# Kernel tuning notes

Measured on AMD Instinct MI355X. Metric: run time of the kernel, lower is better.

## Reference

```python
import jax, jax.numpy as jnp
import numpy as np

NEG_SLOPE = 0.2

def leaky_relu(x):
    return jnp.where(x >= 0, x, NEG_SLOPE * x)

def conv1x1(x, w, b):
    # x: [n,c,h,w], w: [o,c], b: [o]
    return jnp.einsum('nchw,oc->nohw', x, w) + b[None, :, None, None]

def setup_inputs() -> dict:
    key = jax.random.key(0)
    ks = jax.random.split(key, 7)
    n, c, h, w = 4, 64, 80, 80
    scale = 1.0 / np.sqrt(c)
    return {
        'x': jax.random.normal(ks[0], (n, c, h, w), dtype=jnp.float32),
        'w1': jax.random.normal(ks[1], (c, c), dtype=jnp.float32) * scale,
        'b1': jax.random.normal(ks[2], (c,), dtype=jnp.float32) * 0.01,
        'w2': jax.random.normal(ks[3], (c, c), dtype=jnp.float32) * scale,
        'b2': jax.random.normal(ks[4], (c,), dtype=jnp.float32) * 0.01,
        'w3': jax.random.normal(ks[5], (c, c), dtype=jnp.float32) * scale,
        'b3': jax.random.normal(ks[6], (c,), dtype=jnp.float32) * 0.01,
    }

def reference(x, w1, b1, w2, b2, w3, b3):
    n, c, h, w = x.shape
    e1 = leaky_relu(conv1x1(x, w1, b1))  # [n,c,h,w]
    e2 = leaky_relu(conv1x1(x, w2, b2))
    asm = leaky_relu(conv1x1(x, w3, b3))
    # q: [n, hw, c]; k: [n, c, hw]
    q = e1.transpose(0, 2, 3, 1).reshape(n, h * w, c)
    k = e2.reshape(n, c, h * w)
    score = jax.nn.softmax(jnp.matmul(q, k), axis=2)  # [n, hw, hw]
    v = asm.reshape(n, c, h * w).transpose(0, 2, 1)   # [n, hw, c]
    out = jnp.matmul(score, v)                        # [n, hw, c]
    return out.transpose(0, 2, 1).reshape(n, c, h, w)
```

## Files before the change

kernel.cpp:

```cpp
#include <hip/hip_runtime.h>


typedef __attribute__((ext_vector_type(8))) unsigned short us8;
typedef __attribute__((ext_vector_type(4))) unsigned short us4;
typedef __attribute__((ext_vector_type(8))) __bf16 bf16x8;
typedef __attribute__((ext_vector_type(16))) float f32x16;

#define HW 6400
#define L2E 1.44269504088896340736f
#define SHIFT 32.0f
#define KS 4
#define ITERS 25

union V8 { us8 s; us4 h[2]; bf16x8 b; };

__device__ __forceinline__ unsigned short f32_to_bf16(float f) {
  unsigned u = __float_as_uint(f);
  u += 0x7fffu + ((u >> 16) & 1u);
  return (unsigned short)(u >> 16);
}
__device__ __forceinline__ float bf16_bits_to_f32(unsigned short u) {
  return __uint_as_float(((unsigned)u) << 16);
}
__device__ __forceinline__ bf16x8 ldsfrag(const unsigned short* p) {
  V8 r;
  r.h[0] = *(const us4*)p;
  r.h[1] = *(const us4*)(p + 4);
  return r.b;
}

__global__ __launch_bounds__(256, 4) void conv_kernel(
    const float* __restrict__ x,
    const float* __restrict__ w1, const float* __restrict__ b1,
    const float* __restrict__ w2, const float* __restrict__ b2,
    const float* __restrict__ w3, const float* __restrict__ b3,
    unsigned short* __restrict__ Qg, unsigned short* __restrict__ Kg,
    unsigned short* __restrict__ Vg) {
  __shared__ __align__(16) float xs[64 * 68];
  const int t = threadIdx.x;
  const int n = blockIdx.y;
  const int p0 = blockIdx.x * 64;
  const int k = blockIdx.z;

  {
    const int c = t >> 2, part = t & 3;
    const float* src = x + ((size_t)(n * 64 + c) * HW + p0 + part * 16);
    float* dst = xs + c * 68 + part * 16;
#pragma unroll
    for (int i = 0; i < 4; ++i)
      *(float4*)(dst + i * 4) = *(const float4*)(src + i * 4);
  }

  const float* wm = (k == 0) ? w1 : (k == 1) ? w2 : w3;
  const float* bm = (k == 0) ? b1 : (k == 1) ? b2 : b3;
  const int p = t & 63;
  const int cg = __builtin_amdgcn_readfirstlane(t >> 6);

  __syncthreads();

  float acc[16];
#pragma unroll
  for (int i = 0; i < 16; ++i) acc[i] = bm[cg * 16 + i];
#pragma unroll
  for (int c4 = 0; c4 < 16; ++c4) {
    const float xv0 = xs[(c4 * 4 + 0) * 68 + p];
    const float xv1 = xs[(c4 * 4 + 1) * 68 + p];
    const float xv2 = xs[(c4 * 4 + 2) * 68 + p];
    const float xv3 = xs[(c4 * 4 + 3) * 68 + p];
#pragma unroll
    for (int i = 0; i < 16; ++i) {
      const float4 wv = *(const float4*)(wm + (cg * 16 + i) * 64 + c4 * 4);
      acc[i] = fmaf(wv.x, xv0, acc[i]);
      acc[i] = fmaf(wv.y, xv1, acc[i]);
      acc[i] = fmaf(wv.z, xv2, acc[i]);
      acc[i] = fmaf(wv.w, xv3, acc[i]);
    }
  }
#pragma unroll
  for (int i = 0; i < 16; ++i)
    acc[i] = fmaxf(acc[i], 0.f) + 0.2f * fminf(acc[i], 0.f);

  if (k == 0) {
    unsigned short u[16];
#pragma unroll
    for (int i = 0; i < 16; ++i) u[i] = f32_to_bf16(acc[i] * L2E);
    unsigned short* dst = Qg + (size_t)(n * HW + p0 + p) * 64 + cg * 16;
    us8 a, b;
#pragma unroll
    for (int j = 0; j < 8; ++j) { a[j] = u[j]; b[j] = u[8 + j]; }
    *(us8*)dst = a;
    *(us8*)(dst + 8) = b;
  } else if (k == 1) {
    unsigned short u[16];
#pragma unroll
    for (int i = 0; i < 16; ++i) u[i] = f32_to_bf16(acc[i]);
    unsigned short* dst = Kg + (size_t)(n * HW + p0 + p) * 64 + cg * 16;
    us8 a, b;
#pragma unroll
    for (int j = 0; j < 8; ++j) { a[j] = u[j]; b[j] = u[8 + j]; }
    *(us8*)dst = a;
    *(us8*)(dst + 8) = b;
  } else {
#pragma unroll
    for (int i = 0; i < 16; ++i)
      Vg[(size_t)(n * 64 + cg * 16 + i) * HW + p0 + p] = f32_to_bf16(acc[i]);
  }
}

__global__ __launch_bounds__(256, 3) void attn_kernel(
    const unsigned short* __restrict__ Qg, const unsigned short* __restrict__ Kg,
    const unsigned short* __restrict__ Vg, float* __restrict__ Opart,
    float* __restrict__ Lpart) {
  __shared__ __align__(16) char smem[52224];
  unsigned short* Qs = (unsigned short*)smem;
  unsigned short* Ksh = (unsigned short*)(smem + 17408);
  unsigned short* Vsh = (unsigned short*)(smem + 26112);
  unsigned short* Ps = (unsigned short*)(smem + 34816);
  float* Ot = (float*)smem;

  const int t = threadIdx.x;
  const int w = t >> 6;
  const int lane = t & 63;
  const int l31 = lane & 31;
  const int lh = lane >> 5;
  const int nb = blockIdx.y;
  const int qb = blockIdx.x * 128;
  const int ks = blockIdx.z;
  const int key0 = ks * (HW / KS);

  {
    const unsigned short* src = Qg + (size_t)(nb * HW + qb) * 64 + t * 32;
    unsigned short* dst = Qs + (t >> 1) * 68 + (t & 1) * 32;
#pragma unroll
    for (int i = 0; i < 4; ++i) {
      V8 v; v.s = *(const us8*)(src + i * 8);
      *(us4*)(dst + i * 8) = v.h[0];
      *(us4*)(dst + i * 8 + 4) = v.h[1];
    }
  }
  __syncthreads();

  bf16x8 aQ[4];
#pragma unroll
  for (int kst = 0; kst < 4; ++kst)
    aQ[kst] = ldsfrag(Qs + (w * 32 + l31) * 68 + kst * 16 + lh * 8);

  f32x16 accO[2];
#pragma unroll
  for (int ci = 0; ci < 2; ++ci)
#pragma unroll
    for (int r = 0; r < 16; ++r) accO[ci][r] = 0.f;
  float lpart = 0.f;

  const unsigned short* kbase = Kg + (size_t)nb * HW * 64;
  const unsigned short* vbase = Vg + (size_t)nb * 64 * HW;

  V8 kr0, kr1, vr0, vr1;
  {
    const unsigned short* ksrc = kbase + (size_t)(key0)*64 + t * 16;
    kr0.s = *(const us8*)ksrc;
    kr1.s = *(const us8*)(ksrc + 8);
    const unsigned short* vsrc = vbase + (size_t)(t >> 2) * HW + key0 + (t & 3) * 16;
    vr0.s = *(const us8*)vsrc;
    vr1.s = *(const us8*)(vsrc + 8);
  }

#pragma unroll 1
  for (int jt = 0; jt < ITERS; ++jt) {
    __syncthreads();
    {
      unsigned short* kdst = Ksh + (t >> 2) * 68 + (t & 3) * 16;
      *(us4*)(kdst) = kr0.h[0];
      *(us4*)(kdst + 4) = kr0.h[1];
      *(us4*)(kdst + 8) = kr1.h[0];
      *(us4*)(kdst + 12) = kr1.h[1];
      unsigned short* vdst = Vsh + (t >> 2) * 68 + (t & 3) * 16;
      *(us4*)(vdst) = vr0.h[0];
      *(us4*)(vdst + 4) = vr0.h[1];
      *(us4*)(vdst + 8) = vr1.h[0];
      *(us4*)(vdst + 12) = vr1.h[1];
    }
    __syncthreads();

    if (jt + 1 < ITERS) {
      const unsigned short* ksrc =
          kbase + (size_t)(key0 + (jt + 1) * 64) * 64 + t * 16;
      kr0.s = *(const us8*)ksrc;
      kr1.s = *(const us8*)(ksrc + 8);
      const unsigned short* vsrc =
          vbase + (size_t)(t >> 2) * HW + key0 + (jt + 1) * 64 + (t & 3) * 16;
      vr0.s = *(const us8*)vsrc;
      vr1.s = *(const us8*)(vsrc + 8);
    }

    f32x16 sacc[2];
#pragma unroll
    for (int ni = 0; ni < 2; ++ni)
#pragma unroll
      for (int r = 0; r < 16; ++r) sacc[ni][r] = 0.f;
#pragma unroll
    for (int kst = 0; kst < 4; ++kst) {
      const bf16x8 aK0 = ldsfrag(Ksh + l31 * 68 + kst * 16 + lh * 8);
      const bf16x8 aK1 = ldsfrag(Ksh + (32 + l31) * 68 + kst * 16 + lh * 8);
      sacc[0] = __builtin_amdgcn_mfma_f32_32x32x16_bf16(aK0, aQ[kst], sacc[0], 0, 0, 0);
      sacc[1] = __builtin_amdgcn_mfma_f32_32x32x16_bf16(aK1, aQ[kst], sacc[1], 0, 0, 0);
    }

    unsigned short* prow = Ps + (w * 32 + l31) * 68;
#pragma unroll
    for (int ni = 0; ni < 2; ++ni) {
#pragma unroll
      for (int q = 0; q < 4; ++q) {
        us4 pk;
#pragma unroll
        for (int j = 0; j < 4; ++j) {
          const float pv = __builtin_amdgcn_exp2f(sacc[ni][4 * q + j] - SHIFT);
          const unsigned short u = f32_to_bf16(pv);
          lpart += bf16_bits_to_f32(u);
          pk[j] = u;
        }
        *(us4*)(prow + ni * 32 + 8 * q + 4 * lh) = pk;
      }
    }

#pragma unroll
    for (int kst = 0; kst < 4; ++kst) {
      const bf16x8 ap = ldsfrag(Ps + (w * 32 + l31) * 68 + kst * 16 + lh * 8);
      const bf16x8 bv0 = ldsfrag(Vsh + l31 * 68 + kst * 16 + lh * 8);
      const bf16x8 bv1 = ldsfrag(Vsh + (32 + l31) * 68 + kst * 16 + lh * 8);
      accO[0] = __builtin_amdgcn_mfma_f32_32x32x16_bf16(ap, bv0, accO[0], 0, 0, 0);
      accO[1] = __builtin_amdgcn_mfma_f32_32x32x16_bf16(ap, bv1, accO[1], 0, 0, 0);
    }
  }

  const float lsum = lpart + __shfl_xor(lpart, 32);
  if (lh == 0)
    Lpart[((size_t)ks * 4 + nb) * HW + qb + w * 32 + l31] = lsum;

  __syncthreads();
#pragma unroll
  for (int ci = 0; ci < 2; ++ci)
#pragma unroll
    for (int r = 0; r < 16; ++r)
      Ot[(ci * 32 + l31) * 132 + w * 32 + 4 * lh + (r & 3) + 8 * (r >> 2)] =
          accO[ci][r];
  __syncthreads();
  {
    const int ch = t >> 2, part = t & 3;
    const float* src = Ot + ch * 132 + part * 32;
    float* dst = Opart + ((size_t)ks * 4 + nb) * (64 * HW) + (size_t)ch * HW +
                 qb + part * 32;
#pragma unroll
    for (int i = 0; i < 8; ++i)
      *(float4*)(dst + i * 4) = *(const float4*)(src + i * 4);
  }
}

__global__ __launch_bounds__(256) void combine_kernel(
    const float* __restrict__ Opart, const float* __restrict__ Lpart,
    float* __restrict__ out) {
  const int tid = blockIdx.x * 256 + threadIdx.x;
  const size_t e = (size_t)tid * 4;
  float4 o = {0.f, 0.f, 0.f, 0.f};
#pragma unroll
  for (int ks = 0; ks < KS; ++ks) {
    const float4 v = *(const float4*)(Opart + (size_t)ks * (4 * 64 * HW) + e);
    o.x += v.x; o.y += v.y; o.z += v.z; o.w += v.w;
  }
  const int n = (int)(e / (64 * HW));
  const int p = (int)(e % HW);
  float4 l = {0.f, 0.f, 0.f, 0.f};
#pragma unroll
  for (int ks = 0; ks < KS; ++ks) {
    const float4 v = *(const float4*)(Lpart + ((size_t)ks * 4 + n) * HW + p);
    l.x += v.x; l.y += v.y; l.z += v.z; l.w += v.w;
  }
  float4 r;
  r.x = o.x / l.x; r.y = o.y / l.y; r.z = o.z / l.z; r.w = o.w / l.w;
  *(float4*)(out + e) = r;
}

extern "C" void kernel_launch(void* const* d_in, const int* in_sizes, int n_in,
                              void* d_out, int out_size, void* d_ws, size_t ws_size,
                              hipStream_t stream) {
  const float* x = (const float*)d_in[0];
  const float* w1 = (const float*)d_in[1];
  const float* b1 = (const float*)d_in[2];
  const float* w2 = (const float*)d_in[3];
  const float* b2 = (const float*)d_in[4];
  const float* w3 = (const float*)d_in[5];
  const float* b3 = (const float*)d_in[6];
  float* out = (float*)d_out;

  unsigned short* Q = (unsigned short*)d_ws;
  unsigned short* K = Q + (size_t)4 * HW * 64;
  unsigned short* V = K + (size_t)4 * HW * 64;
  float* Opart = (float*)(V + (size_t)4 * HW * 64);
  float* Lpart = Opart + (size_t)KS * 4 * 64 * HW;

  conv_kernel<<<dim3(100, 4, 3), 256, 0, stream>>>(x, w1, b1, w2, b2, w3, b3,
                                                   Q, K, V);
  attn_kernel<<<dim3(50, 4, KS), 256, 0, stream>>>(Q, K, V, Opart, Lpart);
  combine_kernel<<<1600, 256, 0, stream>>>(Opart, Lpart, out);
}
```

Measured before the change: 166.7 us.

## Double-buffer K/V in LDS and pass P through registers via lane shuffles

The attention kernel now double-buffers K/V tiles in LDS, so each iteration needs one barrier instead of two. The probability tile is no longer written to and read back from LDS; it is packed to bf16 pairs and moved between lane halves with shuffles. Q fragments are loaded straight from global memory into registers, the LDS row stride is padded to 72, and occupancy is raised to 4 blocks per CU. The row sum now uses the fp32 probabilities instead of the rounded bf16 values, and the conv kernel preloads weights per channel group with the outer loop left unrolled once. The changes trade LDS traffic and barriers for register pressure and cross-lane operations, with a small numerical difference in the softmax normalisation.

```diff
diff --git a/kernel.cpp b/kernel.cpp
--- a/kernel.cpp
+++ b/kernel.cpp
@@ -12,21 +12,25 @@
 #define KS 4
 #define ITERS 25
 
-union V8 { us8 s; us4 h[2]; bf16x8 b; };
+union V8 { us8 s; us4 h[2]; bf16x8 b; unsigned u4[4]; };
 
 __device__ __forceinline__ unsigned short f32_to_bf16(float f) {
   unsigned u = __float_as_uint(f);
   u += 0x7fffu + ((u >> 16) & 1u);
   return (unsigned short)(u >> 16);
 }
-__device__ __forceinline__ float bf16_bits_to_f32(unsigned short u) {
-  return __uint_as_float(((unsigned)u) << 16);
-}
-__device__ __forceinline__ bf16x8 ldsfrag(const unsigned short* p) {
-  V8 r;
-  r.h[0] = *(const us4*)p;
-  r.h[1] = *(const us4*)(p + 4);
-  return r.b;
+
+__device__ __forceinline__ unsigned pack_bf16x2(float a, float b) {
+#if __has_builtin(__builtin_amdgcn_cvt_pk_bf16_f32)
+  auto v = __builtin_amdgcn_cvt_pk_bf16_f32(a, b);
+  unsigned u;
+  __builtin_memcpy(&u, &v, 4);
+  return u;
+#else
+  unsigned ua = __float_as_uint(a); ua += 0x7fffu + ((ua >> 16) & 1u);
+  unsigned ub = __float_as_uint(b); ub += 0x7fffu + ((ub >> 16) & 1u);
+  return (ua >> 16) | (ub & 0xffff0000u);
+#endif
 }
 
 __global__ __launch_bounds__(256, 4) void conv_kernel(
@@ -61,19 +65,22 @@
   float acc[16];
 #pragma unroll
   for (int i = 0; i < 16; ++i) acc[i] = bm[cg * 16 + i];
-#pragma unroll
+#pragma unroll 1
   for (int c4 = 0; c4 < 16; ++c4) {
+    float4 wv[16];
+#pragma unroll
+    for (int i = 0; i < 16; ++i)
+      wv[i] = *(const float4*)(wm + (cg * 16 + i) * 64 + c4 * 4);
     const float xv0 = xs[(c4 * 4 + 0) * 68 + p];
     const float xv1 = xs[(c4 * 4 + 1) * 68 + p];
     const float xv2 = xs[(c4 * 4 + 2) * 68 + p];
     const float xv3 = xs[(c4 * 4 + 3) * 68 + p];
 #pragma unroll
     for (int i = 0; i < 16; ++i) {
-      const float4 wv = *(const float4*)(wm + (cg * 16 + i) * 64 + c4 * 4);
-      acc[i] = fmaf(wv.x, xv0, acc[i]);
-      acc[i] = fmaf(wv.y, xv1, acc[i]);
-      acc[i] = fmaf(wv.z, xv2, acc[i]);
-      acc[i] = fmaf(wv.w, xv3, acc[i]);
+      acc[i] = fmaf(wv[i].x, xv0, acc[i]);
+      acc[i] = fmaf(wv[i].y, xv1, acc[i]);
+      acc[i] = fmaf(wv[i].z, xv2, acc[i]);
+      acc[i] = fmaf(wv[i].w, xv3, acc[i]);
     }
   }
 #pragma unroll
@@ -107,15 +114,11 @@
   }
 }
 
-__global__ __launch_bounds__(256, 3) void attn_kernel(
+__global__ __launch_bounds__(256, 4) void attn_kernel(
     const unsigned short* __restrict__ Qg, const unsigned short* __restrict__ Kg,
     const unsigned short* __restrict__ Vg, float* __restrict__ Opart,
     float* __restrict__ Lpart) {
-  __shared__ __align__(16) char smem[52224];
-  unsigned short* Qs = (unsigned short*)smem;
-  unsigned short* Ksh = (unsigned short*)(smem + 17408);
-  unsigned short* Vsh = (unsigned short*)(smem + 26112);
-  unsigned short* Ps = (unsigned short*)(smem + 34816);
+  __shared__ __align__(16) char smem[36864];
   float* Ot = (float*)smem;
 
   const int t = threadIdx.x;
@@ -128,108 +131,106 @@
   const int ks = blockIdx.z;
   const int key0 = ks * (HW / KS);
 
+  const unsigned short* qrow =
+      Qg + (size_t)(nb * HW + qb + w * 32 + l31) * 64 + lh * 8;
+  V8 aQ[4];
+#pragma unroll
+  for (int kst = 0; kst < 4; ++kst) aQ[kst].s = *(const us8*)(qrow + kst * 16);
+
+  f32x16 accO0, accO1;
+#pragma unroll
+  for (int r = 0; r < 16; ++r) { accO0[r] = 0.f; accO1[r] = 0.f; }
+  float lpart = 0.f;
+
+  const int soff = (t >> 2) * 72 + (t & 3) * 16;
+  const unsigned short* ksrc =
+      Kg + (size_t)nb * HW * 64 + (size_t)(key0 + (t >> 2)) * 64 + (t & 3) * 16;
+  const unsigned short* vsrc =
+      Vg + (size_t)nb * 64 * HW + (size_t)(t >> 2) * HW + key0 + (t & 3) * 16;
+
+  V8 kr0, kr1, vr0, vr1;
+  kr0.s = *(const us8*)ksrc;
+  kr1.s = *(const us8*)(ksrc + 8);
+  vr0.s = *(const us8*)vsrc;
+  vr1.s = *(const us8*)(vsrc + 8);
   {
-    const unsigned short* src = Qg + (size_t)(nb * HW + qb) * 64 + t * 32;
-    unsigned short* dst = Qs + (t >> 1) * 68 + (t & 1) * 32;
-#pragma unroll
-    for (int i = 0; i < 4; ++i) {
-      V8 v; v.s = *(const us8*)(src + i * 8);
-      *(us4*)(dst + i * 8) = v.h[0];
-      *(us4*)(dst + i * 8 + 4) = v.h[1];
-    }
+    unsigned short* kd = (unsigned short*)smem + soff;
+    unsigned short* vd = (unsigned short*)(smem + 18432) + soff;
+    *(us8*)kd = kr0.s; *(us8*)(kd + 8) = kr1.s;
+    *(us8*)vd = vr0.s; *(us8*)(vd + 8) = vr1.s;
   }
   __syncthreads();
-
-  bf16x8 aQ[4];
-#pragma unroll
-  for (int kst = 0; kst < 4; ++kst)
-    aQ[kst] = ldsfrag(Qs + (w * 32 + l31) * 68 + kst * 16 + lh * 8);
-
-  f32x16 accO[2];
-#pragma unroll
-  for (int ci = 0; ci < 2; ++ci)
-#pragma unroll
-    for (int r = 0; r < 16; ++r) accO[ci][r] = 0.f;
-  float lpart = 0.f;
-
-  const unsigned short* kbase = Kg + (size_t)nb * HW * 64;
-  const unsigned short* vbase = Vg + (size_t)nb * 64 * HW;
-
-  V8 kr0, kr1, vr0, vr1;
-  {
-    const unsigned short* ksrc = kbase + (size_t)(key0)*64 + t * 16;
-    kr0.s = *(const us8*)ksrc;
-    kr1.s = *(const us8*)(ksrc + 8);
-    const unsigned short* vsrc = vbase + (size_t)(t >> 2) * HW + key0 + (t & 3) * 16;
-    vr0.s = *(const us8*)vsrc;
-    vr1.s = *(const us8*)(vsrc + 8);
-  }
 
 #pragma unroll 1
   for (int jt = 0; jt < ITERS; ++jt) {
-    __syncthreads();
-    {
-      unsigned short* kdst = Ksh + (t >> 2) * 68 + (t & 3) * 16;
-      *(us4*)(kdst) = kr0.h[0];
-      *(us4*)(kdst + 4) = kr0.h[1];
-      *(us4*)(kdst + 8) = kr1.h[0];
-      *(us4*)(kdst + 12) = kr1.h[1];
-      unsigned short* vdst = Vsh + (t >> 2) * 68 + (t & 3) * 16;
-      *(us4*)(vdst) = vr0.h[0];
-      *(us4*)(vdst + 4) = vr0.h[1];
-      *(us4*)(vdst + 8) = vr1.h[0];
-      *(us4*)(vdst + 12) = vr1.h[1];
-    }
-    __syncthreads();
-
-    if (jt + 1 < ITERS) {
-      const unsigned short* ksrc =
-          kbase + (size_t)(key0 + (jt + 1) * 64) * 64 + t * 16;
-      kr0.s = *(const us8*)ksrc;
-      kr1.s = *(const us8*)(ksrc + 8);
-      const unsigned short* vsrc =
-          vbase + (size_t)(t >> 2) * HW + key0 + (jt + 1) * 64 + (t & 3) * 16;
-      vr0.s = *(const us8*)vsrc;
-      vr1.s = *(const us8*)(vsrc + 8);
-    }
-
-    f32x16 sacc[2];
-#pragma unroll
-    for (int ni = 0; ni < 2; ++ni)
-#pragma unroll
-      for (int r = 0; r < 16; ++r) sacc[ni][r] = 0.f;
+    const int b = jt & 1;
+    const unsigned short* Kc = (const unsigned short*)(smem + b * 9216);
+    const unsigned short* Vc = (const unsigned short*)(smem + 18432 + b * 9216);
+    const bool more = (jt + 1 < ITERS);
+
+    if (more) {
+      kr0.s = *(const us8*)(ksrc + (jt + 1) * 4096);
+      kr1.s = *(const us8*)(ksrc + (jt + 1) * 4096 + 8);
+      vr0.s = *(const us8*)(vsrc + (jt + 1) * 64);
+      vr1.s = *(const us8*)(vsrc + (jt + 1) * 64 + 8);
+    }
+
+    uint2 pkq[2][4];
+#pragma unroll
+    for (int ni = 0; ni < 2; ++ni) {
+      f32x16 sacc;
+#pragma unroll
+      for (int r = 0; r < 16; ++r) sacc[r] = 0.f;
+#pragma unroll
+      for (int kst = 0; kst < 4; ++kst) {
+        V8 ak;
+        ak.s = *(const us8*)(Kc + (ni * 32 + l31) * 72 + kst * 16 + lh * 8);
+        sacc = __builtin_amdgcn_mfma_f32_32x32x16_bf16(ak.b, aQ[kst].b, sacc,
+                                                       0, 0, 0);
+      }
+#pragma unroll
+      for (int g = 0; g < 4; ++g) {
+        const float p0 = __builtin_amdgcn_exp2f(sacc[4 * g + 0] - SHIFT);
+        const float p1 = __builtin_amdgcn_exp2f(sacc[4 * g + 1] - SHIFT);
+        const float p2 = __builtin_amdgcn_exp2f(sacc[4 * g + 2] - SHIFT);
+        const float p3 = __builtin_amdgcn_exp2f(sacc[4 * g + 3] - SHIFT);
+        lpart += (p0 + p1) + (p2 + p3);
+        pkq[ni][g].x = pack_bf16x2(p0, p1);
+        pkq[ni][g].y = pack_bf16x2(p2, p3);
+      }
+    }
+
 #pragma unroll
     for (int kst = 0; kst < 4; ++kst) {
-      const bf16x8 aK0 = ldsfrag(Ksh + l31 * 68 + kst * 16 + lh * 8);
-      const bf16x8 aK1 = ldsfrag(Ksh + (32 + l31) * 68 + kst * 16 + lh * 8);
-      sacc[0] = __builtin_amdgcn_mfma_f32_32x32x16_bf16(aK0, aQ[kst], sacc[0], 0, 0, 0);
-      sacc[1] = __builtin_amdgcn_mfma_f32_32x32x16_bf16(aK1, aQ[kst], sacc[1], 0, 0, 0);
-    }
-
-    unsigned short* prow = Ps + (w * 32 + l31) * 68;
-#pragma unroll
-    for (int ni = 0; ni < 2; ++ni) {
-#pragma unroll
-      for (int q = 0; q < 4; ++q) {
-        us4 pk;
-#pragma unroll
-        for (int j = 0; j < 4; ++j) {
-          const float pv = __builtin_amdgcn_exp2f(sacc[ni][4 * q + j] - SHIFT);
-          const unsigned short u = f32_to_bf16(pv);
-          lpart += bf16_bits_to_f32(u);
-          pk[j] = u;
-        }
-        *(us4*)(prow + ni * 32 + 8 * q + 4 * lh) = pk;
-      }
-    }
-
-#pragma unroll
-    for (int kst = 0; kst < 4; ++kst) {
-      const bf16x8 ap = ldsfrag(Ps + (w * 32 + l31) * 68 + kst * 16 + lh * 8);
-      const bf16x8 bv0 = ldsfrag(Vsh + l31 * 68 + kst * 16 + lh * 8);
-      const bf16x8 bv1 = ldsfrag(Vsh + (32 + l31) * 68 + kst * 16 + lh * 8);
-      accO[0] = __builtin_amdgcn_mfma_f32_32x32x16_bf16(ap, bv0, accO[0], 0, 0, 0);
-      accO[1] = __builtin_amdgcn_mfma_f32_32x32x16_bf16(ap, bv1, accO[1], 0, 0, 0);
+      const int ni = kst >> 1;
+      const int gb = 2 * (kst & 1);
+      const uint2 qa = pkq[ni][gb];
+      const uint2 qb2 = pkq[ni][gb + 1];
+      uint2 send;
+      send.x = lh ? qa.x : qb2.x;
+      send.y = lh ? qa.y : qb2.y;
+      uint2 recv;
+      recv.x = __shfl_xor(send.x, 32);
+      recv.y = __shfl_xor(send.y, 32);
+      const uint2 keep = {lh ? qb2.x : qa.x, lh ? qb2.y : qa.y};
+      V8 ap;
+      ap.u4[0] = lh ? recv.x : keep.x;
+      ap.u4[1] = lh ? recv.y : keep.y;
+      ap.u4[2] = lh ? keep.x : recv.x;
+      ap.u4[3] = lh ? keep.y : recv.y;
+      V8 bv0, bv1;
+      bv0.s = *(const us8*)(Vc + l31 * 72 + kst * 16 + lh * 8);
+      bv1.s = *(const us8*)(Vc + (32 + l31) * 72 + kst * 16 + lh * 8);
+      accO0 = __builtin_amdgcn_mfma_f32_32x32x16_bf16(ap.b, bv0.b, accO0, 0, 0, 0);
+      accO1 = __builtin_amdgcn_mfma_f32_32x32x16_bf16(ap.b, bv1.b, accO1, 0, 0, 0);
+    }
+
+    if (more) {
+      unsigned short* kd = (unsigned short*)(smem + (1 - b) * 9216) + soff;
+      unsigned short* vd = (unsigned short*)(smem + 18432 + (1 - b) * 9216) + soff;
+      *(us8*)kd = kr0.s; *(us8*)(kd + 8) = kr1.s;
+      *(us8*)vd = vr0.s; *(us8*)(vd + 8) = vr1.s;
+      __syncthreads();
     }
   }
 
@@ -239,11 +240,11 @@
 
   __syncthreads();
 #pragma unroll
-  for (int ci = 0; ci < 2; ++ci)
-#pragma unroll
-    for (int r = 0; r < 16; ++r)
-      Ot[(ci * 32 + l31) * 132 + w * 32 + 4 * lh + (r & 3) + 8 * (r >> 2)] =
-          accO[ci][r];
+  for (int r = 0; r < 16; ++r) {
+    const int m = w * 32 + 8 * (r >> 2) + 4 * lh + (r & 3);
+    Ot[l31 * 132 + m] = accO0[r];
+    Ot[(32 + l31) * 132 + m] = accO1[r];
+  }
   __syncthreads();
   {
     const int ch = t >> 2, part = t & 3;
```

Result: no change. 167.7 us (+0.6%).
